# Optimization experiments

Hardware: AMD Instinct MI355X
Metric: run time of the kernel (lower is better)

The kernel has to match this reference:

```python
import jax, jax.numpy as jnp
import numpy as np

B, L, DM, E, N, R, S = 2, 1024, 512, 1024, 16, 32, 64
BN_SCALE = float(1.0 / np.sqrt(1.0 + 1e-5))  # eval-mode BatchNorm1d with default running stats


def _ssm(x, Wx, bx, Wdt, bdt, A_log, D):
    # x: [B,L,E] -> Mamba selective scan output [B,L,E]
    dbc = x @ Wx.T + bx                                   # [B,L,R+2N]
    delta = jax.nn.softplus(dbc[..., :R] @ Wdt.T + bdt)   # [B,L,E]
    Bm = dbc[..., R:R + N]                                # [B,L,N]
    Cm = dbc[..., R + N:]                                 # [B,L,N]
    A = -jnp.exp(A_log)                                   # [E,N]
    dA = jnp.exp(delta[..., None] * A)                    # [B,L,E,N]
    dBx = delta[..., None] * Bm[:, :, None, :] * x[..., None]

    def comb(c1, c2):
        a1, b1 = c1
        a2, b2 = c2
        return a1 * a2, b1 * a2 + b2

    _, h = jax.lax.associative_scan(comb, (dA, dBx), axis=1)  # [B,L,E,N]
    return jnp.einsum('blen,bln->ble', h, Cm) + D * x


def _gmask_idx(length, batch):
    ref = (length + 1) // 2
    idx = jnp.arange(length, dtype=jnp.float32)
    sigma = jnp.abs(idx - ref).mean()
    w = jnp.exp(-0.5 * (idx - ref) ** 2 / sigma ** 2)
    w = w / w.sum()
    return jnp.broadcast_to(w, (batch, length))


def _gmask_vec(seq):
    length = seq.shape[1]
    ref = seq[:, (length + 1) // 2, :]
    d = jnp.linalg.norm(seq - ref[:, None, :], axis=2)    # [B,L]
    sigma = d.mean(axis=1, keepdims=True)
    w = jnp.exp(-0.5 * (d / sigma) ** 2)
    return w / w.sum(axis=1, keepdims=True)


def _spatial_attn(x, w, b):
    # x: [B,L,C]; SpatialAttention: returns weighted map in [B,C,L] layout
    xt = jnp.swapaxes(x, 1, 2)                            # [B,C,L]
    fmap = (w[0] * xt.max(axis=1) + w[1] * xt.mean(axis=1) + b) * BN_SCALE
    wmap = jax.nn.sigmoid(jax.nn.relu(fmap))[:, None, :]  # [B,1,L]
    return xt * wmap                                      # [B,C,L]


def _forward(x, W_in_x, b_in_x, W_in_z, b_in_z, convf_w, convf_b, convb_w, convb_b,
             Wx_f, bx_f, Wdt_f, bdt_f, A_log_f, D_f,
             Wx_b, bx_b, Wdt_b, bdt_b, A_log_b, D_b,
             W_cat, b_cat, sa_w, sa_b, wA_f, wV_f,
             W_proj, b_proj, W_Bi, b_Bi, tf_w, tf_b, W_out, b_out):
    b_, l_, _ = x.shape
    xi = x @ W_in_x.T + b_in_x                            # [B,L,E]
    z = x @ W_in_z.T + b_in_z                             # [B,L,E]
    # depthwise conv1d with kernel_size=1 == per-channel affine
    x_f = jax.nn.silu(xi * convf_w + convf_b)
    x_b = jax.nn.silu(jnp.flip(xi, axis=1) * convb_w + convb_b)
    y_f = jnp.tanh(_ssm(x_f, Wx_f, bx_f, Wdt_f, bdt_f, A_log_f, D_f))
    y_b = jnp.tanh(_ssm(x_b, Wx_b, bx_b, Wdt_b, bdt_b, A_log_b, D_b))
    gi = _gmask_idx(l_, b_)
    mf = jax.nn.softmax(gi * _gmask_vec(y_f), axis=1)
    mb = jax.nn.softmax(gi * _gmask_vec(y_b), axis=1)
    y_cat = jnp.concatenate([y_f * mf[..., None],
                             y_b * jnp.flip(mb[..., None], axis=1)], axis=-1)
    y = y_cat @ W_cat.T + b_cat                           # [B,L,E]
    m = jax.nn.softmax(gi * _gmask_vec(y_cat), axis=1)
    y = y * m[..., None]
    yw = _spatial_attn(y, sa_w, sa_b)                     # [B,E,L]
    y = jnp.swapaxes(yw, 1, 2)                            # [B,L,E]
    # STL tokenizer (forward direction weights)
    Aw = jax.nn.softmax(jnp.swapaxes(y @ wA_f.T, 1, 2), axis=-1)  # [B,S,L]
    u = Aw @ (y @ wV_f)                                   # [B,S,E]
    # z branch: adaptive average pool L -> S (L % S == 0), then SiLU
    zp = jax.nn.silu(jnp.swapaxes(z, 1, 2).reshape(b_, E, S, l_ // S).mean(-1))
    zt = jnp.swapaxes(zp, 1, 2)                           # [B,S,E]
    # TokenFuser -- faithful to original's .view-based memory reinterpretation
    Y = (u.reshape(b_, E, S) @ W_proj.T + b_proj).reshape(b_, S, E)
    Bw = jax.nn.sigmoid(zt @ W_Bi.T + b_Bi)               # [B,S,S]
    BwY = Bw @ Y                                          # [B,S,E]
    xj = _spatial_attn(zt, tf_w, tf_b).reshape(b_, S, E)  # view (reshape), not transpose
    out = BwY + xj
    return jnp.tanh(out @ W_out.T + b_out)                # [B,S,DM]


def setup_inputs():
    ks = jax.random.split(jax.random.key(0), 24)
    g = lambda i, shape, s=0.02: jax.random.normal(ks[i], shape, dtype=jnp.float32) * s
    A_log = jnp.log(jnp.tile(jnp.arange(1, N + 1, dtype=jnp.float32), (E, 1)))
    return dict(
        x=jax.random.normal(ks[0], (B, L, DM), dtype=jnp.float32),
        W_in_x=g(1, (E, DM)), b_in_x=jnp.zeros((E,), jnp.float32),
        W_in_z=g(2, (E, DM)), b_in_z=jnp.zeros((E,), jnp.float32),
        convf_w=1.0 + g(3, (E,)), convf_b=jnp.zeros((E,), jnp.float32),
        convb_w=1.0 + g(4, (E,)), convb_b=jnp.zeros((E,), jnp.float32),
        Wx_f=g(5, (R + 2 * N, E)), bx_f=jnp.zeros((R + 2 * N,), jnp.float32),
        Wdt_f=g(6, (E, R)), bdt_f=jnp.full((E,), -4.0, jnp.float32),
        A_log_f=A_log, D_f=jnp.ones((E,), jnp.float32),
        Wx_b=g(7, (R + 2 * N, E)), bx_b=jnp.zeros((R + 2 * N,), jnp.float32),
        Wdt_b=g(8, (E, R)), bdt_b=jnp.full((E,), -4.0, jnp.float32),
        A_log_b=A_log, D_b=jnp.ones((E,), jnp.float32),
        W_cat=g(9, (E, 2 * E)), b_cat=jnp.zeros((E,), jnp.float32),
        sa_w=g(10, (2,), 0.5), sa_b=jnp.zeros((), jnp.float32),
        wA_f=g(11, (S, E), 0.05), wV_f=g(12, (E, E), 0.02),
        W_proj=g(13, (S, S), 0.1), b_proj=jnp.zeros((S,), jnp.float32),
        W_Bi=g(14, (S, E)), b_Bi=jnp.zeros((S,), jnp.float32),
        tf_w=g(15, (2,), 0.5), tf_b=jnp.zeros((), jnp.float32),
        W_out=g(16, (DM, E)), b_out=jnp.zeros((DM,), jnp.float32),
    )


def reference(x, W_in_x, b_in_x, W_in_z, b_in_z, convf_w, convf_b, convb_w, convb_b,
              Wx_f, bx_f, Wdt_f, bdt_f, A_log_f, D_f,
              Wx_b, bx_b, Wdt_b, bdt_b, A_log_b, D_b,
              W_cat, b_cat, sa_w, sa_b, wA_f, wV_f,
              W_proj, b_proj, W_Bi, b_Bi, tf_w, tf_b, W_out, b_out):
    return _forward(x, W_in_x, b_in_x, W_in_z, b_in_z, convf_w, convf_b, convb_w, convb_b,
                    Wx_f, bx_f, Wdt_f, bdt_f, A_log_f, D_f,
                    Wx_b, bx_b, Wdt_b, bdt_b, A_log_b, D_b,
                    W_cat, b_cat, sa_w, sa_b, wA_f, wV_f,
                    W_proj, b_proj, W_Bi, b_Bi, tf_w, tf_b, W_out, b_out)
```

## Files before the change

kernel.cpp:

```cpp
#include <hip/hip_runtime.h>
#include <math.h>

#define DEVI static __device__ __forceinline__

namespace {

constexpr float BN_SCALE_C = 0.9999950000374997f;

typedef __bf16 bf8v __attribute__((ext_vector_type(8)));
typedef float f4v __attribute__((ext_vector_type(4)));

DEVI float sigmoidf_(float x){ return 1.0f/(1.0f+expf(-x)); }
DEVI float siluf_(float x){ return x/(1.0f+expf(-x)); }
DEVI float softplusf_(float x){ return fmaxf(x,0.0f) + log1pf(expf(-fabsf(x))); }

DEVI unsigned short f2bf(float f){
  union{float f; unsigned int u;} v; v.f=f;
  unsigned int r = v.u + 0x7fffu + ((v.u>>16)&1u);
  return (unsigned short)(r>>16);
}
DEVI float bf2f(unsigned short u){
  union{unsigned int u; float f;} v; v.u = ((unsigned int)u)<<16;
  return v.f;
}

DEVI float bredw_sum(float v, float* sh){
  #pragma unroll
  for (int o=32;o;o>>=1) v += __shfl_xor(v, o);
  __syncthreads();
  if ((threadIdx.x&63)==0) sh[threadIdx.x>>6] = v;
  __syncthreads();
  return sh[0]+sh[1]+sh[2]+sh[3];
}
DEVI float bredw_max(float v, float* sh){
  #pragma unroll
  for (int o=32;o;o>>=1) v = fmaxf(v, __shfl_xor(v, o));
  __syncthreads();
  if ((threadIdx.x&63)==0) sh[threadIdx.x>>6] = v;
  __syncthreads();
  return fmaxf(fmaxf(sh[0],sh[1]), fmaxf(sh[2],sh[3]));
}

DEVI void gld_lds16(const unsigned short* g, unsigned short* l){
  __builtin_amdgcn_global_load_lds(
      (const __attribute__((address_space(1))) unsigned int*)(g),
      (__attribute__((address_space(3))) unsigned int*)(l), 16, 0, 0);
}

DEVI void stage_tile64(const unsigned short* __restrict__ Ak,
                       const unsigned short* __restrict__ Bk,
                       size_t lda, size_t ldb,
                       unsigned short* As, unsigned short* Bs,
                       int w, int lane)
{
  #pragma unroll
  for (int i=0;i<2;++i){
    int seg = (w<<1) + i;
    int row = (seg<<3) + (lane>>3);
    int c   = (lane & 7) ^ (row & 7);
    gld_lds16(Ak + (size_t)row*lda + (c<<3), As + (seg<<9));
    gld_lds16(Bk + (size_t)row*ldb + (c<<3), Bs + (seg<<9));
  }
}

DEVI void gemm_core(const unsigned short* __restrict__ Ag,
                    const unsigned short* __restrict__ Bg,
                    size_t lda, size_t ldb, int ksteps,
                    unsigned short* As, unsigned short* Bs, f4v (&acc)[2][2])
{
  const int tid = threadIdx.x;
  const int lane = tid & 63, w = tid >> 6;
  const int wr = w >> 1, wc = w & 1;
  const int l15 = lane & 15, l4 = lane >> 4;

  int cur = 0;
  stage_tile64(Ag, Bg, lda, ldb, As, Bs, w, lane);
  asm volatile("s_waitcnt vmcnt(0)" ::: "memory");
  __syncthreads();
  for (int ks = 0; ks < ksteps; ++ks){
    unsigned short* Asc = As + (cur<<12);
    unsigned short* Bsc = Bs + (cur<<12);
    if (ks+1 < ksteps)
      stage_tile64(Ag + (size_t)(ks+1)*64, Bg + (size_t)(ks+1)*64, lda, ldb,
                   As + ((cur^1)<<12), Bs + ((cur^1)<<12), w, lane);
    #pragma unroll
    for (int kk=0;kk<2;++kk){
      int cb = (kk<<2) + l4;
      bf8v af[2], bfv[2];
      #pragma unroll
      for (int mi=0;mi<2;++mi){
        int row = (wr<<5)+(mi<<4)+l15;
        af[mi] = *(const bf8v*)(Asc + (row<<6) + ((cb^(row&7))<<3));
      }
      #pragma unroll
      for (int ni=0;ni<2;++ni){
        int row = (wc<<5)+(ni<<4)+l15;
        bfv[ni] = *(const bf8v*)(Bsc + (row<<6) + ((cb^(row&7))<<3));
      }
      #pragma unroll
      for (int mi=0;mi<2;++mi)
        #pragma unroll
        for (int ni=0;ni<2;++ni)
          acc[mi][ni] = __builtin_amdgcn_mfma_f32_16x16x32_bf16(af[mi], bfv[ni], acc[mi][ni], 0,0,0);
    }
    asm volatile("s_waitcnt vmcnt(0)" ::: "memory");
    __syncthreads();
    cur ^= 1;
  }
}

__global__ __launch_bounds__(256) void gemm_bf16_k(
    const unsigned short* __restrict__ A, const unsigned short* __restrict__ Bt,
    const float* __restrict__ bias, float* __restrict__ C,
    int N, int K,
    const unsigned short* __restrict__ Bt2, const float* __restrict__ bias2, long sC)
{
  __shared__ unsigned short As[8192], Bs[8192];
  if (Bt2 && blockIdx.z){ Bt = Bt2; bias = bias2; C += sC; }
  const int m0 = blockIdx.y<<6, n0 = blockIdx.x<<6;
  f4v acc[2][2] = {};
  gemm_core(A + (size_t)m0*K, Bt + (size_t)n0*K, K, K, K>>6, As, Bs, acc);
  const int lane = threadIdx.x & 63, w = threadIdx.x >> 6;
  const int wr = w>>1, wc = w&1, l15 = lane&15, l4 = lane>>4;
  #pragma unroll
  for (int mi=0;mi<2;++mi)
    #pragma unroll
    for (int ni=0;ni<2;++ni){
      int col = n0 + (wc<<5) + (ni<<4) + l15;
      float bv = bias ? bias[col] : 0.f;
      #pragma unroll
      for (int r=0;r<4;++r){
        int rowg = m0 + (wr<<5) + (mi<<4) + (l4<<2) + r;
        C[(size_t)rowg*N + col] = acc[mi][ni][r] + bv;
      }
    }
}

__global__ __launch_bounds__(256) void gemm_bf16_splitk_k(
    const unsigned short* __restrict__ A, const unsigned short* __restrict__ Bt,
    float* __restrict__ P, int N, int K, int KC, int mshift, long sB)
{
  __shared__ unsigned short As[8192], Bs[8192];
  const int m0 = blockIdx.y<<6, n0 = blockIdx.x<<6, ch = blockIdx.z;
  const unsigned short* Bb = Bt + (size_t)(m0>>mshift)*sB;
  f4v acc[2][2] = {};
  gemm_core(A + (size_t)m0*K + (size_t)ch*KC, Bb + (size_t)n0*K + (size_t)ch*KC,
            K, K, KC>>6, As, Bs, acc);
  const size_t Mtot = (size_t)gridDim.y<<6;
  float* Pc = P + (size_t)ch*Mtot*N;
  const int lane = threadIdx.x & 63, w = threadIdx.x >> 6;
  const int wr = w>>1, wc = w&1, l15 = lane&15, l4 = lane>>4;
  #pragma unroll
  for (int mi=0;mi<2;++mi)
    #pragma unroll
    for (int ni=0;ni<2;++ni){
      int col = n0 + (wc<<5) + (ni<<4) + l15;
      #pragma unroll
      for (int r=0;r<4;++r){
        int rowg = m0 + (wr<<5) + (mi<<4) + (l4<<2) + r;
        Pc[(size_t)rowg*N + col] = acc[mi][ni][r];
      }
    }
}

template<int ACT>
__global__ __launch_bounds__(256) void sk_reduce_k(
    const float* __restrict__ P, const float* __restrict__ b0,
    int nshift, int MN, int nch, float* __restrict__ out)
{
  int i = blockIdx.x*256 + threadIdx.x;
  if (i >= MN) return;
  float s = 0.f;
  for (int c=0;c<nch;++c) s += P[(size_t)c*MN + i];
  if (b0) s += b0[i & ((1<<nshift)-1)];
  if (ACT==3) s = tanhf(s);
  out[i] = s;
}

__global__ __launch_bounds__(256) void skred_bf_k(const float* __restrict__ P,
                                                  unsigned short* __restrict__ out)
{
  int i = (blockIdx.x*256 + threadIdx.x)<<2;
  float4 s0 = *(const float4*)(P + i);
  float4 s1 = *(const float4*)(P + 131072 + i);
  float4 s2 = *(const float4*)(P + 262144 + i);
  float4 s3 = *(const float4*)(P + 393216 + i);
  union{unsigned short u[4]; uint2 p;} o;
  o.u[0] = f2bf(s0.x+s1.x+s2.x+s3.x);
  o.u[1] = f2bf(s0.y+s1.y+s2.y+s3.y);
  o.u[2] = f2bf(s0.z+s1.z+s2.z+s3.z);
  o.u[3] = f2bf(s0.w+s1.w+s2.w+s3.w);
  *(uint2*)(out + i) = o.p;
}

__global__ __launch_bounds__(256) void castall_k(
    const float* __restrict__ s0, unsigned short* __restrict__ d0, int n0,
    const float* __restrict__ s1, unsigned short* __restrict__ d1, int n1,
    const float* __restrict__ s2, unsigned short* __restrict__ d2, int n2,
    const float* __restrict__ s3, unsigned short* __restrict__ d3, int n3,
    const float* __restrict__ s4, unsigned short* __restrict__ d4, int n4,
    const float* __restrict__ s5, unsigned short* __restrict__ d5, int n5,
    const float* __restrict__ s6, unsigned short* __restrict__ d6, int n6,
    const float* __restrict__ s7, unsigned short* __restrict__ d7, int n7)
{
  int i = (blockIdx.x*256 + threadIdx.x)*4;
  const float* s; unsigned short* d;
  if (i < n0){ s = s0; d = d0; }
  else if ((i -= n0) < n1){ s = s1; d = d1; }
  else if ((i -= n1) < n2){ s = s2; d = d2; }
  else if ((i -= n2) < n3){ s = s3; d = d3; }
  else if ((i -= n3) < n4){ s = s4; d = d4; }
  else if ((i -= n4) < n5){ s = s5; d = d5; }
  else if ((i -= n5) < n6){ s = s6; d = d6; }
  else if ((i -= n6) < n7){ s = s7; d = d7; }
  else return;
  float4 v = *(const float4*)(s + i);
  union{ unsigned short u[4]; uint2 p; } o;
  o.u[0]=f2bf(v.x); o.u[1]=f2bf(v.y); o.u[2]=f2bf(v.z); o.u[3]=f2bf(v.w);
  *(uint2*)(d + i) = o.p;
}

__global__ __launch_bounds__(256) void castTw_k(const float* __restrict__ wV,
    unsigned short* __restrict__ wVT,
    const float* __restrict__ Wdt_f, const float* __restrict__ Wdt_b,
    float* __restrict__ WdtT)
{
  __shared__ float t[32][33];
  int by = blockIdx.y, bx = blockIdx.x;
  int tx = threadIdx.x & 31, ty = threadIdx.x >> 5;
  if (by < 32){
    #pragma unroll
    for (int r=0;r<4;++r){
      int row = by*32 + ty + r*8;
      t[ty + r*8][tx] = wV[(long)row*1024 + bx*32 + tx];
    }
    __syncthreads();
    #pragma unroll
    for (int r=0;r<4;++r){
      int row = bx*32 + ty + r*8;
      wVT[(long)row*1024 + by*32 + tx] = f2bf(t[tx][ty + r*8]);
    }
  } else {
    int dir = by - 32;
    const float* src = dir ? Wdt_b : Wdt_f;
    float* dst = WdtT + (dir<<15);
    #pragma unroll
    for (int r=0;r<4;++r){
      int row = bx*32 + ty + r*8;
      t[ty + r*8][tx] = src[(long)row*32 + tx];
    }
    __syncthreads();
    #pragma unroll
    for (int r=0;r<4;++r){
      int c = ty + r*8;
      dst[(long)c*1024 + bx*32 + tx] = t[tx][c];
    }
  }
}

__global__ __launch_bounds__(256) void castTbf_k(const unsigned short* __restrict__ src,
                                                 unsigned short* __restrict__ dst)
{
  __shared__ unsigned short t[32][33];
  size_t bo = (size_t)blockIdx.z << 20;
  int bx = blockIdx.x, by = blockIdx.y;
  int tx = threadIdx.x & 31, ty = threadIdx.x >> 5;
  #pragma unroll
  for (int r=0;r<4;++r){
    int row = by*32 + ty + r*8;
    t[ty + r*8][tx] = src[bo + (long)row*1024 + bx*32 + tx];
  }
  __syncthreads();
  #pragma unroll
  for (int r=0;r<4;++r){
    int row = bx*32 + ty + r*8;
    dst[bo + (long)row*1024 + by*32 + tx] = t[tx][ty + r*8];
  }
}

__global__ __launch_bounds__(256) void convzt_k(const float* __restrict__ xi, const float* __restrict__ z,
    const float* __restrict__ cfw, const float* __restrict__ cfb,
    const float* __restrict__ cbw, const float* __restrict__ cbb,
    float* __restrict__ xf, float* __restrict__ xb, unsigned short* __restrict__ xfb_bf,
    float* __restrict__ ztb)
{
  int bx = blockIdx.x, t = threadIdx.x;
  if (bx < 2048){
    int base = (bx*256 + t) << 2;
    int e = base & 1023;
    int bl = base >> 10; int l = bl & 1023, b = bl >> 10;
    float4 cw = *(const float4*)(cfw + e);
    float4 cb = *(const float4*)(cfb + e);
    float4 xv = *(const float4*)(xi + base);
    float4 vf;
    vf.x = siluf_(fmaf(xv.x, cw.x, cb.x));
    vf.y = siluf_(fmaf(xv.y, cw.y, cb.y));
    vf.z = siluf_(fmaf(xv.z, cw.z, cb.z));
    vf.w = siluf_(fmaf(xv.w, cw.w, cb.w));
    *(float4*)(xf + base) = vf;
    union{unsigned short u[4]; uint2 p;} o;
    o.u[0]=f2bf(vf.x); o.u[1]=f2bf(vf.y); o.u[2]=f2bf(vf.z); o.u[3]=f2bf(vf.w);
    *(uint2*)(xfb_bf + base) = o.p;
    int jb = (((b<<10) + (1023-l))<<10) + e;
    float4 cw2 = *(const float4*)(cbw + e);
    float4 cb2 = *(const float4*)(cbb + e);
    float4 xw = *(const float4*)(xi + jb);
    float4 vb;
    vb.x = siluf_(fmaf(xw.x, cw2.x, cb2.x));
    vb.y = siluf_(fmaf(xw.y, cw2.y, cb2.y));
    vb.z = siluf_(fmaf(xw.z, cw2.z, cb2.z));
    vb.w = siluf_(fmaf(xw.w, cw2.w, cb2.w));
    *(float4*)(xb + base) = vb;
    union{unsigned short u[4]; uint2 p;} o2;
    o2.u[0]=f2bf(vb.x); o2.u[1]=f2bf(vb.y); o2.u[2]=f2bf(vb.z); o2.u[3]=f2bf(vb.w);
    *(uint2*)(xfb_bf + 2097152 + base) = o2.p;
  } else {
    int base = ((bx-2048)*256 + t) << 2;
    int e = base & 1023; int bs = base >> 10; int s = bs & 63; int b = bs >> 6;
    const float* zp = z + (((long)((b<<10)+(s<<4)))<<10) + e;
    float4 sm = {0.f,0.f,0.f,0.f};
    #pragma unroll
    for (int j=0;j<16;++j){
      float4 v = *(const float4*)(zp + ((long)j<<10));
      sm.x += v.x; sm.y += v.y; sm.z += v.z; sm.w += v.w;
    }
    float4 o;
    o.x = siluf_(sm.x*(1.f/16.f)); o.y = siluf_(sm.y*(1.f/16.f));
    o.z = siluf_(sm.z*(1.f/16.f)); o.w = siluf_(sm.w*(1.f/16.f));
    *(float4*)(ztb + base) = o;
  }
}

__global__ __launch_bounds__(256) void dbcdelta_k(
    const float* __restrict__ Pd,
    const float* __restrict__ bx_f, const float* __restrict__ bx_b,
    const float* __restrict__ WdtT,
    const float* __restrict__ bdt_f, const float* __restrict__ bdt_b,
    float* __restrict__ dbcF, float* __restrict__ delta)
{
  __shared__ float sdbc[8][64];
  const int t = threadIdx.x;
  const int r0 = blockIdx.x * 8;
  const int dir = r0 >> 11;
  const float* bx  = dir ? bx_b  : bx_f;
  const float* bdt = dir ? bdt_b : bdt_f;
  const float* WT  = WdtT + (dir<<15);
  for (int idx=t; idx<512; idx+=256){
    int r = idx>>6, c = idx&63;
    long a = (long)(r0+r)*64 + c;
    float s = Pd[a] + Pd[262144+a] + Pd[524288+a] + Pd[786432+a] + bx[c];
    sdbc[r][c] = s;
    dbcF[a] = s;
  }
  __syncthreads();
  const int c0 = t << 2;
  float4 bv = *(const float4*)(bdt + c0);
  float4 acc[8];
  #pragma unroll
  for (int r=0;r<8;++r) acc[r] = bv;
  #pragma unroll
  for (int k=0;k<32;++k){
    float4 w = *(const float4*)(WT + (k<<10) + c0);
    #pragma unroll
    for (int r=0;r<8;++r){
      float a = sdbc[r][k];
      acc[r].x = fmaf(a, w.x, acc[r].x);
      acc[r].y = fmaf(a, w.y, acc[r].y);
      acc[r].z = fmaf(a, w.z, acc[r].z);
      acc[r].w = fmaf(a, w.w, acc[r].w);
    }
  }
  #pragma unroll
  for (int r=0;r<8;++r){
    float4 o;
    o.x = softplusf_(acc[r].x); o.y = softplusf_(acc[r].y);
    o.z = softplusf_(acc[r].z); o.w = softplusf_(acc[r].w);
    *(float4*)(delta + (long)(r0+r)*1024 + c0) = o;
  }
}

__global__ __launch_bounds__(256) void ssm_chunk_k(
    const float* __restrict__ xs0, const float* __restrict__ dl0,
    const float* __restrict__ dbc0, const float* __restrict__ A_log_f,
    const float* __restrict__ A_log_b,
    float* __restrict__ pA0, float* __restrict__ hend0)
{
  const int dir = blockIdx.y;
  const float* xs   = xs0  + (size_t)dir*2097152;
  const float* delta= dl0  + (size_t)dir*2097152;
  const float* dbc  = dbc0 + (size_t)dir*131072;
  const float* A_log= dir ? A_log_b : A_log_f;
  float* pA   = pA0   + (size_t)dir*1048576;
  float* hend = hend0 + (size_t)dir*1048576;

  __shared__ float sB[32][16];
  int g = blockIdx.x*256 + threadIdx.x;
  int e = g & 1023;
  int bc = g >> 10;
  int c = bc & 31, b = bc >> 5;
  for (int i=threadIdx.x; i<512; i+=256){
    int l=i>>4, n=i&15;
    sB[l][n] = dbc[(((b<<10) + (c<<5) + l)<<6) + 32 + n];
  }
  __syncthreads();
  float An[16];
  #pragma unroll
  for (int n=0;n<16;++n) An[n] = -__expf(A_log[(e<<4)+n]);
  float h[16], p[16];
  #pragma unroll
  for (int n=0;n<16;++n){ h[n]=0.0f; p[n]=1.0f; }
  long base = ((long)((b<<10) + (c<<5)))*1024 + e;
  for (int l=0;l<32;++l){
    float dl = delta[base + ((long)l<<10)];
    float xv = xs[base + ((long)l<<10)];
    float dx = dl*xv;
    #pragma unroll
    for (int n=0;n<16;++n){
      float a = __expf(dl*An[n]);
      h[n] = fmaf(a, h[n], dx*sB[l][n]);
      p[n] *= a;
    }
  }
  long ob = ((long)((b<<5)+c)<<4)*1024 + e;
  #pragma unroll
  for (int n=0;n<16;++n){ pA[ob + ((long)n<<10)] = p[n]; hend[ob + ((long)n<<10)] = h[n]; }
}

__global__ __launch_bounds__(256) void ssm_carry_k(
    const float* __restrict__ pA, const float* __restrict__ hend, float* __restrict__ Hc)
{
  int i = blockIdx.x*256 + threadIdx.x;
  int e = i & 1023, n = (i>>10)&15, b = (i>>14)&1, dir = (i>>15)&1;
  const float* pAd = pA   + (size_t)dir*1048576;
  const float* hd  = hend + (size_t)dir*1048576;
  float* Hd        = Hc   + (size_t)dir*1048576;
// ... 100 lines not shown
    float* __restrict__ mfG, float* __restrict__ mbG, float* __restrict__ mvG)
{
  __shared__ float mfs[1024], mbs[1024], sh[4];
  const int b = blockIdx.x, t = threadIdx.x;
  const float nf512 = nrm[(b<<10)+512];
  const float nb512 = nrm[2048+(b<<10)+512];
  float gi[4], nf[4], pf[4], nb[4], pb[4];
  float gs = 0.f;
  #pragma unroll
  for (int i=0;i<4;++i){
    int l = t + (i<<8);
    float q = (float)(l-512) * (1.0f/256.0f);
    gi[i] = __expf(-0.5f*q*q); gs += gi[i];
    nf[i] = nrm[(b<<10)+l];      pf[i] = dotv[(b<<10)+l];
    nb[i] = nrm[2048+(b<<10)+l]; pb[i] = dotv[2048+(b<<10)+l];
  }
  float gsum = bredw_sum(gs, sh);
  float mf[4], mb[4], d[4];
  #pragma unroll
  for (int i=0;i<4;++i) d[i] = sqrtf(fmaxf(nf[i] - 2.f*pf[i] + nf512, 0.f));
  softmask(d, gi, gsum, sh, mf);
  #pragma unroll
  for (int i=0;i<4;++i) d[i] = sqrtf(fmaxf(nb[i] - 2.f*pb[i] + nb512, 0.f));
  softmask(d, gi, gsum, sh, mb);
  #pragma unroll
  for (int i=0;i<4;++i){
    int l = t + (i<<8);
    mfs[l] = mf[i]; mbs[l] = mb[i];
    mfG[(b<<10)+l] = mf[i]; mbG[(b<<10)+l] = mb[i];
  }
  __syncthreads();
  const float mf512 = mfs[512], mb511 = mbs[511];
  #pragma unroll
  for (int i=0;i<4;++i){
    int l = t + (i<<8);
    float mbf = mbs[1023-l];
    float dc2 = mf[i]*mf[i]*nf[i] - 2.f*mf[i]*mf512*pf[i] + mf512*mf512*nf512
              + mbf*mbf*nb[i]     - 2.f*mbf*mb511*pb[i]   + mb511*mb511*nb512;
    d[i] = sqrtf(fmaxf(dc2, 0.f));
  }
  float mv[4];
  softmask(d, gi, gsum, sh, mv);
  #pragma unroll
  for (int i=0;i<4;++i) mvG[(b<<10)+t+(i<<8)] = mv[i];
}

__global__ __launch_bounds__(256) void ycat_k(const float* __restrict__ yf, const float* __restrict__ yb,
    const float* __restrict__ mf, const float* __restrict__ mb, unsigned short* __restrict__ yc)
{
  int base = (blockIdx.x*256 + threadIdx.x) << 2;
  int e = base & 1023; int bl = base >> 10; int l = bl & 1023, b = bl >> 10;
  float mfv = mf[bl];
  float mbv = mb[(b<<10) + (1023-l)];
  float4 vf = *(const float4*)(yf + base);
  float4 vb = *(const float4*)(yb + base);
  long r = (long)bl*2048;
  union{unsigned short u[4]; uint2 p;} o;
  o.u[0]=f2bf(vf.x*mfv); o.u[1]=f2bf(vf.y*mfv); o.u[2]=f2bf(vf.z*mfv); o.u[3]=f2bf(vf.w*mfv);
  *(uint2*)(yc + r + e) = o.p;
  union{unsigned short u[4]; uint2 p;} o2;
  o2.u[0]=f2bf(vb.x*mbv); o2.u[1]=f2bf(vb.y*mbv); o2.u[2]=f2bf(vb.z*mbv); o2.u[3]=f2bf(vb.w*mbv);
  *(uint2*)(yc + r + 1024 + e) = o2.p;
}

__global__ __launch_bounds__(256) void rowscale_k(const float* __restrict__ y, const float* __restrict__ m,
    const float* __restrict__ sw, const float* __restrict__ sb, unsigned short* __restrict__ yo)
{
  __shared__ float sh[4];
  int row = blockIdx.x;
  float mv = m[row];
  float4 v = ((const float4*)(y + (long)row*1024))[threadIdx.x];
  v.x *= mv; v.y *= mv; v.z *= mv; v.w *= mv;
  float mx = fmaxf(fmaxf(v.x,v.y), fmaxf(v.z,v.w));
  float sm = v.x+v.y+v.z+v.w;
  float rmax = bredw_max(mx, sh);
  float rsum = bredw_sum(sm, sh);
  float fmap = (sw[0]*rmax + sw[1]*(rsum*(1.0f/1024.0f)) + sb[0])*BN_SCALE_C;
  float sc = sigmoidf_(fmaxf(fmap, 0.0f));
  union{unsigned short u[4]; uint2 p;} o;
  o.u[0]=f2bf(v.x*sc); o.u[1]=f2bf(v.y*sc); o.u[2]=f2bf(v.z*sc); o.u[3]=f2bf(v.w*sc);
  *(uint2*)(yo + (long)row*1024 + (threadIdx.x<<2)) = o.p;
}

__global__ __launch_bounds__(256) void awsm_part_k(const float* __restrict__ P2,
                                                   unsigned short* __restrict__ Aw)
{
  __shared__ float sh[4];
  int bs = blockIdx.x; int b = bs >> 6, s = bs & 63;
  float v[4]; float mx=-1e30f;
  #pragma unroll
  for(int i=0;i<4;++i){
    int l = threadIdx.x+(i<<8);
    long a = (long)((b<<10)+l)*64 + s;
    float sv = 0.f;
    #pragma unroll
    for (int ch=0; ch<8; ++ch) sv += P2[(long)ch*131072 + a];
    v[i] = sv; mx = fmaxf(mx, sv);
  }
  mx = bredw_max(mx, sh);
  float sm=0.0f;
  #pragma unroll
  for(int i=0;i<4;++i){ v[i]=__expf(v[i]-mx); sm+=v[i]; }
  sm = bredw_sum(sm, sh);
  float inv = 1.0f/sm;
  #pragma unroll
  for(int i=0;i<4;++i){ int l=threadIdx.x+(i<<8); Aw[(((b<<6)+s)<<10)+l] = f2bf(v[i]*inv); }
}

__global__ __launch_bounds__(256) void upbw_k(const float* __restrict__ P2u,
    const float* __restrict__ W_proj, const float* __restrict__ b_proj,
    const float* __restrict__ zt, const float* __restrict__ W_Bi,
    const float* __restrict__ b_Bi, const float* __restrict__ tw,
    const float* __restrict__ tb,
    float* __restrict__ Yp, float* __restrict__ Bw, float* __restrict__ gz)
{
  __shared__ float a[1024];
  __shared__ float sh[4];
  const int t = threadIdx.x;
  if (blockIdx.x < 256){
    const int r0 = blockIdx.x*8;
    for (int idx=t; idx<512; idx+=256){
      int r = idx>>6, sp = idx&63;
      long ad = (long)(r0+r)*64 + sp;
      float s = P2u[ad] + P2u[131072+ad] + P2u[262144+ad] + P2u[393216+ad];
      a[idx] = s;
    }
    __syncthreads();
    int r = t >> 5, c = t & 31;
    const float* ar = a + (r<<6);
    float acc1 = b_proj[c], acc2 = b_proj[c+32];
    for (int sp=0; sp<64; ++sp){
      float av = ar[sp];
      acc1 = fmaf(av, W_proj[c*64+sp], acc1);
      acc2 = fmaf(av, W_proj[(c+32)*64+sp], acc2);
    }
    long row = r0 + r;
    Yp[row*64 + c] = acc1;
    Yp[row*64 + c + 32] = acc2;
  } else {
    const int row = blockIdx.x - 256;
    float4 zv = ((const float4*)(zt + (long)row*1024))[t];
    *(float4*)(a + (t<<2)) = zv;
    float mx = fmaxf(fmaxf(zv.x,zv.y), fmaxf(zv.z,zv.w));
    float sm = zv.x+zv.y+zv.z+zv.w;
    mx = bredw_max(mx, sh);
    sm = bredw_sum(sm, sh);
    if (t==0){
      float f = (tw[0]*mx + tw[1]*(sm*(1.0f/1024.0f)) + tb[0])*BN_SCALE_C;
      gz[row] = sigmoidf_(fmaxf(f,0.0f));
    }
    __syncthreads();
    int col = t >> 2, q = t & 3;
    const float4* wp = (const float4*)(W_Bi + (long)col*1024 + q*256);
    const float4* zp = (const float4*)(a + q*256);
    float acc = 0.f;
    for (int i=0;i<64;++i){
      float4 w = wp[i], zc = zp[i];
      acc += w.x*zc.x + w.y*zc.y + w.z*zc.z + w.w*zc.w;
    }
    acc += __shfl_xor(acc, 1);
    acc += __shfl_xor(acc, 2);
    if (q==0) Bw[(long)row*64 + col] = sigmoidf_(acc + b_Bi[col]);
  }
}

__global__ __launch_bounds__(256) void o_k(const float* __restrict__ Bw,
    const float* __restrict__ Yp, const float* __restrict__ zt,
    const float* __restrict__ gz, unsigned short* __restrict__ O_bf)
{
  __shared__ float bwrow[64];
  const int t = threadIdx.x;
  const int bs = blockIdx.x; const int b = bs >> 6, s = bs & 63;
  if (t < 64) bwrow[t] = Bw[(long)bs*64 + t];
  __syncthreads();
  const int e0 = t << 2;
  const float* yb = Yp + (long)b*65536 + e0;
  float4 acc = {0.f,0.f,0.f,0.f};
  for (int s2=0; s2<64; ++s2){
    float f = bwrow[s2];
    float4 y = *(const float4*)(yb + ((long)s2<<10));
    acc.x = fmaf(f,y.x,acc.x); acc.y = fmaf(f,y.y,acc.y);
    acc.z = fmaf(f,y.z,acc.z); acc.w = fmaf(f,y.w,acc.w);
  }
  int ez = (s<<4) + (e0>>6);
  float o4[4] = {acc.x, acc.y, acc.z, acc.w};
  union{unsigned short u[4]; uint2 p;} o;
  #pragma unroll
  for (int k=0;k<4;++k){
    int sz = (e0&63) + k;
    float xj = zt[(((long)((b<<6)+sz))<<10) + ez] * gz[(b<<6)+sz];
    o.u[k] = f2bf(o4[k] + xj);
  }
  *(uint2*)(O_bf + (long)bs*1024 + e0) = o.p;
}

}

extern "C" void kernel_launch(void* const* d_in, const int* in_sizes, int n_in,
                              void* d_out, int out_size, void* d_ws, size_t ws_size,
                              hipStream_t stream)
{
  (void)in_sizes; (void)n_in; (void)out_size; (void)ws_size;
  const float* x      = (const float*)d_in[0];
  const float* W_in_x = (const float*)d_in[1];
  const float* b_in_x = (const float*)d_in[2];
  const float* W_in_z = (const float*)d_in[3];
  const float* b_in_z = (const float*)d_in[4];
  const float* cfw    = (const float*)d_in[5];
  const float* cfb    = (const float*)d_in[6];
  const float* cbw    = (const float*)d_in[7];
  const float* cbb    = (const float*)d_in[8];
  const float* Wx_f   = (const float*)d_in[9];
  const float* bx_f   = (const float*)d_in[10];
  const float* Wdt_f  = (const float*)d_in[11];
  const float* bdt_f  = (const float*)d_in[12];
  const float* A_log_f= (const float*)d_in[13];
  const float* D_f    = (const float*)d_in[14];
  const float* Wx_b   = (const float*)d_in[15];
  const float* bx_b   = (const float*)d_in[16];
  const float* Wdt_b  = (const float*)d_in[17];
  const float* bdt_b  = (const float*)d_in[18];
  const float* A_log_b= (const float*)d_in[19];
  const float* D_b    = (const float*)d_in[20];
  const float* W_cat  = (const float*)d_in[21];
  const float* b_cat  = (const float*)d_in[22];
  const float* sa_w   = (const float*)d_in[23];
  const float* sa_b   = (const float*)d_in[24];
  const float* wA_f   = (const float*)d_in[25];
  const float* wV_f   = (const float*)d_in[26];
  const float* W_proj = (const float*)d_in[27];
  const float* b_proj = (const float*)d_in[28];
  const float* W_Bi   = (const float*)d_in[29];
  const float* b_Bi   = (const float*)d_in[30];
  const float* tf_w   = (const float*)d_in[31];
  const float* tf_b   = (const float*)d_in[32];
  const float* W_out  = (const float*)d_in[33];
  const float* b_out  = (const float*)d_in[34];
  float* out = (float*)d_out;
  float* ws  = (float*)d_ws;

  const size_t M1 = 1u<<20;
  float* xi = ws;
  float* pA = ws;
  unsigned short* ycat_bf = (unsigned short*)ws;
  float* z = ws + 2*M1;
  float* hend = ws + 2*M1;
  float* ybufF = ws + 2*M1;
  float* xf = ws + 4*M1;
  unsigned short* ybuf_bf = (unsigned short*)(ws + 4*M1);
  float* xb = ws + 6*M1;
  unsigned short* ybufT_bf = (unsigned short*)(ws + 6*M1);
  float* yf = ws + 8*M1;
  float* yb = ws + 10*M1;
  float* P2 = ws + 10*M1;
  float* P2b = P2 + 524288;
  unsigned short* xfxb_bf = (unsigned short*)(ws + 12*M1);
  float* deltaF = ws + 12*M1;
  float* Pd = ws + 16*M1;
  unsigned short* x_bf = (unsigned short*)(ws + 17*M1);
  float* Hc = ws + 16*M1;
  float* dbcF = ws + 18*M1;
  size_t woff = 18*M1 + 262144;
  unsigned short* Winx_bf = (unsigned short*)(ws + woff); woff += 262144;
  unsigned short* Winz_bf = (unsigned short*)(ws + woff); woff += 262144;
  unsigned short* Wcat_bf = (unsigned short*)(ws + woff); woff += M1;
  unsigned short* wVT_bf  = (unsigned short*)(ws + woff); woff += 524288;
  unsigned short* wA_bf   = (unsigned short*)(ws + woff); woff += 32768;
  unsigned short* Wx_bf   = (unsigned short*)(ws + woff); woff += 65536;
  unsigned short* Wout_bf = (unsigned short*)(ws + woff); woff += 262144;
  float* WdtT = ws + woff; woff += 65536;
  float* ztb  = ws + woff; woff += 131072;
  float* nrm  = ws + woff; woff += 4096;
  float* dotv = ws + woff; woff += 4096;
  float* mfG  = ws + woff; woff += 2048;
  float* mbG  = ws + woff; woff += 2048;
  float* mvG  = ws + woff; woff += 2048;
  float* gz   = ws + woff; woff += 256;
  unsigned short* Aw_bf = (unsigned short*)(ws + woff); woff += 65536;
  unsigned short* uR_bf = (unsigned short*)(ws + woff); woff += 65536;
  float* Yp   = ws + woff; woff += 131072;
  float* Bw   = ws + woff; woff += 8192;
  unsigned short* O_bf = (unsigned short*)(ws + woff); woff += 65536;

  dim3 blk(256);

  castall_k<<<4800,blk,0,stream>>>(x, x_bf, 1048576,
                                   W_in_x, Winx_bf, 524288,
                                   W_in_z, Winz_bf, 524288,
                                   W_cat, Wcat_bf, 2097152,
                                   wA_f, wA_bf, 65536,
                                   Wx_f, Wx_bf, 65536,
                                   Wx_b, Wx_bf + 65536, 65536,
                                   W_out, Wout_bf, 524288);
  castTw_k<<<dim3(32,34),blk,0,stream>>>(wV_f, wVT_bf, Wdt_f, Wdt_b, WdtT);

  gemm_bf16_k<<<dim3(16,32,2),blk,0,stream>>>(x_bf, Winx_bf, b_in_x, xi, 1024, 512,
                                              Winz_bf, b_in_z, (long)(2*M1));
  convzt_k<<<2176,blk,0,stream>>>(xi, z, cfw,cfb,cbw,cbb, xf, xb, xfxb_bf, ztb);

  gemm_bf16_splitk_k<<<dim3(1,64,4),blk,0,stream>>>(xfxb_bf, Wx_bf, Pd, 64, 1024, 256, 11, 65536);
  dbcdelta_k<<<512,blk,0,stream>>>(Pd, bx_f, bx_b, WdtT, bdt_f, bdt_b, dbcF, deltaF);

  ssm_chunk_k<<<dim3(256,2),blk,0,stream>>>(xf, deltaF, dbcF, A_log_f, A_log_b, pA, hend);
  ssm_carry_k<<<256,blk,0,stream>>>(pA, hend, Hc);
  ssm_out_k<<<dim3(256,2),blk,0,stream>>>(xf, deltaF, dbcF, A_log_f, A_log_b, Hc, D_f, D_b, yf);

  stats_k<<<4096,blk,0,stream>>>(yf, nrm, dotv);
  mask2_k<<<2,blk,0,stream>>>(nrm, dotv, mfG, mbG, mvG);
  ycat_k<<<2048,blk,0,stream>>>(yf, yb, mfG, mbG, ycat_bf);

  gemm_bf16_k<<<dim3(16,32,1),blk,0,stream>>>(ycat_bf, Wcat_bf, b_cat, ybufF, 1024, 2048,
                                              nullptr, nullptr, 0);
  rowscale_k<<<2048,blk,0,stream>>>(ybufF, mvG, sa_w, sa_b, ybuf_bf);

  gemm_bf16_splitk_k<<<dim3(1,32,8),blk,0,stream>>>(ybuf_bf, wA_bf, P2, 64, 1024, 128, 31, 0);
  awsm_part_k<<<128,blk,0,stream>>>(P2, Aw_bf);
  castTbf_k<<<dim3(32,32,2),blk,0,stream>>>(ybuf_bf, ybufT_bf);
  gemm_bf16_splitk_k<<<dim3(16,2,4),blk,0,stream>>>(Aw_bf, ybufT_bf, P2, 1024, 1024, 256, 6, 1048576);
  skred_bf_k<<<128,blk,0,stream>>>(P2, uR_bf);
  gemm_bf16_splitk_k<<<dim3(16,2,4),blk,0,stream>>>(uR_bf, wVT_bf, P2b, 1024, 1024, 256, 31, 0);

  upbw_k<<<384,blk,0,stream>>>(P2b, W_proj, b_proj, ztb, W_Bi, b_Bi, tf_w, tf_b, Yp, Bw, gz);
  o_k<<<128,blk,0,stream>>>(Bw, Yp, ztb, gz, O_bf);

  gemm_bf16_splitk_k<<<dim3(8,2,8),blk,0,stream>>>(O_bf, Wout_bf, P2, 512, 1024, 128, 31, 0);
  sk_reduce_k<3><<<256,blk,0,stream>>>(P2, b_out, 9, 65536, 8, out);
}
```

Before: 216.3 us.

## Replace split-K GEMMs with full-K GEMMs using fused epilogues and merge transpose kernels

Removes the split-K partial-sum buffers and their reduce kernels. Each GEMM now computes the full K in one launch and applies bias, bf16 conversion or tanh in its epilogue. The weight transposes are folded into the cast kernel and the ybuf transpose into the softmax kernel, reducing the number of kernel launches and intermediate memory traffic. The trade-off is much smaller grids for several GEMMs, which lowers parallelism on a wide GPU.

```diff
diff --git a/kernel.cpp b/kernel.cpp
--- a/kernel.cpp
+++ b/kernel.cpp
@@ -18,10 +18,6 @@
   union{float f; unsigned int u;} v; v.f=f;
   unsigned int r = v.u + 0x7fffu + ((v.u>>16)&1u);
   return (unsigned short)(r>>16);
-}
-DEVI float bf2f(unsigned short u){
-  union{unsigned int u; float f;} v; v.u = ((unsigned int)u)<<16;
-  return v.f;
 }
 
 DEVI float bredw_sum(float v, float* sh){
@@ -109,17 +105,21 @@
   }
 }
 
+template<int EPI>
 __global__ __launch_bounds__(256) void gemm_bf16_k(
     const unsigned short* __restrict__ A, const unsigned short* __restrict__ Bt,
-    const float* __restrict__ bias, float* __restrict__ C,
+    const float* __restrict__ bias, void* __restrict__ Cout,
     int N, int K,
-    const unsigned short* __restrict__ Bt2, const float* __restrict__ bias2, long sC)
+    const unsigned short* __restrict__ Bt2, const float* __restrict__ bias2, long sC,
+    int mshift, long sB)
 {
   __shared__ unsigned short As[8192], Bs[8192];
-  if (Bt2 && blockIdx.z){ Bt = Bt2; bias = bias2; C += sC; }
+  float* Cf = (float*)Cout;
+  if (Bt2 && blockIdx.z){ Bt = Bt2; bias = bias2; Cf += sC; }
   const int m0 = blockIdx.y<<6, n0 = blockIdx.x<<6;
+  const unsigned short* Bb = Bt + (size_t)(m0>>mshift)*sB;
   f4v acc[2][2] = {};
-  gemm_core(A + (size_t)m0*K, Bt + (size_t)n0*K, K, K, K>>6, As, Bs, acc);
+  gemm_core(A + (size_t)m0*K, Bb + (size_t)n0*K, K, K, K>>6, As, Bs, acc);
   const int lane = threadIdx.x & 63, w = threadIdx.x >> 6;
   const int wr = w>>1, wc = w&1, l15 = lane&15, l4 = lane>>4;
   #pragma unroll
@@ -127,70 +127,46 @@
     #pragma unroll
     for (int ni=0;ni<2;++ni){
       int col = n0 + (wc<<5) + (ni<<4) + l15;
-      float bv = bias ? bias[col] : 0.f;
+      float bv = (EPI!=1 && bias) ? bias[col] : 0.f;
       #pragma unroll
       for (int r=0;r<4;++r){
         int rowg = m0 + (wr<<5) + (mi<<4) + (l4<<2) + r;
-        C[(size_t)rowg*N + col] = acc[mi][ni][r] + bv;
+        float v = acc[mi][ni][r] + bv;
+        if (EPI==1){
+          ((unsigned short*)Cout)[(size_t)rowg*N + col] = f2bf(v);
+        } else {
+          if (EPI==2) v = tanhf(v);
+          Cf[(size_t)rowg*N + col] = v;
+        }
       }
     }
 }
 
-__global__ __launch_bounds__(256) void gemm_bf16_splitk_k(
-    const unsigned short* __restrict__ A, const unsigned short* __restrict__ Bt,
-    float* __restrict__ P, int N, int K, int KC, int mshift, long sB)
+__global__ __launch_bounds__(256) void gemm_dbc_k(
+    const unsigned short* __restrict__ A, const unsigned short* __restrict__ Wx_bf,
+    const float* __restrict__ bx_f, const float* __restrict__ bx_b,
+    float* __restrict__ dbcF)
 {
   __shared__ unsigned short As[8192], Bs[8192];
-  const int m0 = blockIdx.y<<6, n0 = blockIdx.x<<6, ch = blockIdx.z;
-  const unsigned short* Bb = Bt + (size_t)(m0>>mshift)*sB;
+  const int m0 = blockIdx.y<<6;
+  const int dir = m0 >> 11;
   f4v acc[2][2] = {};
-  gemm_core(A + (size_t)m0*K + (size_t)ch*KC, Bb + (size_t)n0*K + (size_t)ch*KC,
-            K, K, KC>>6, As, Bs, acc);
-  const size_t Mtot = (size_t)gridDim.y<<6;
-  float* Pc = P + (size_t)ch*Mtot*N;
+  gemm_core(A + (size_t)m0*1024, Wx_bf + (size_t)dir*65536, 1024, 1024, 16, As, Bs, acc);
+  const float* bx = dir ? bx_b : bx_f;
   const int lane = threadIdx.x & 63, w = threadIdx.x >> 6;
   const int wr = w>>1, wc = w&1, l15 = lane&15, l4 = lane>>4;
   #pragma unroll
   for (int mi=0;mi<2;++mi)
     #pragma unroll
     for (int ni=0;ni<2;++ni){
-      int col = n0 + (wc<<5) + (ni<<4) + l15;
+      int col = (wc<<5) + (ni<<4) + l15;
+      float bv = bx[col];
       #pragma unroll
       for (int r=0;r<4;++r){
         int rowg = m0 + (wr<<5) + (mi<<4) + (l4<<2) + r;
-        Pc[(size_t)rowg*N + col] = acc[mi][ni][r];
+        dbcF[(size_t)rowg*64 + col] = acc[mi][ni][r] + bv;
       }
     }
-}
-
-template<int ACT>
-__global__ __launch_bounds__(256) void sk_reduce_k(
-    const float* __restrict__ P, const float* __restrict__ b0,
-    int nshift, int MN, int nch, float* __restrict__ out)
-{
-  int i = blockIdx.x*256 + threadIdx.x;
-  if (i >= MN) return;
-  float s = 0.f;
-  for (int c=0;c<nch;++c) s += P[(size_t)c*MN + i];
-  if (b0) s += b0[i & ((1<<nshift)-1)];
-  if (ACT==3) s = tanhf(s);
-  out[i] = s;
-}
-
-__global__ __launch_bounds__(256) void skred_bf_k(const float* __restrict__ P,
-                                                  unsigned short* __restrict__ out)
-{
-  int i = (blockIdx.x*256 + threadIdx.x)<<2;
-  float4 s0 = *(const float4*)(P + i);
-  float4 s1 = *(const float4*)(P + 131072 + i);
-  float4 s2 = *(const float4*)(P + 262144 + i);
-  float4 s3 = *(const float4*)(P + 393216 + i);
-  union{unsigned short u[4]; uint2 p;} o;
-  o.u[0] = f2bf(s0.x+s1.x+s2.x+s3.x);
-  o.u[1] = f2bf(s0.y+s1.y+s2.y+s3.y);
-  o.u[2] = f2bf(s0.z+s1.z+s2.z+s3.z);
-  o.u[3] = f2bf(s0.w+s1.w+s2.w+s3.w);
-  *(uint2*)(out + i) = o.p;
 }
 
 __global__ __launch_bounds__(256) void castall_k(
@@ -201,8 +177,47 @@
     const float* __restrict__ s4, unsigned short* __restrict__ d4, int n4,
     const float* __restrict__ s5, unsigned short* __restrict__ d5, int n5,
     const float* __restrict__ s6, unsigned short* __restrict__ d6, int n6,
-    const float* __restrict__ s7, unsigned short* __restrict__ d7, int n7)
-{
+    const float* __restrict__ s7, unsigned short* __restrict__ d7, int n7,
+    const float* __restrict__ wV, unsigned short* __restrict__ wVT,
+    const float* __restrict__ Wdt_f, const float* __restrict__ Wdt_b,
+    float* __restrict__ WdtT)
+{
+  __shared__ float tsh[32][33];
+  if (blockIdx.x >= 4800){
+    int tb = blockIdx.x - 4800;
+    int tx = threadIdx.x & 31, ty = threadIdx.x >> 5;
+    if (tb < 1024){
+      int by = tb >> 5, bx = tb & 31;
+      #pragma unroll
+      for (int r=0;r<4;++r){
+        int row = by*32 + ty + r*8;
+        tsh[ty + r*8][tx] = wV[(long)row*1024 + bx*32 + tx];
+      }
+      __syncthreads();
+      #pragma unroll
+      for (int r=0;r<4;++r){
+        int row = bx*32 + ty + r*8;
+        wVT[(long)row*1024 + by*32 + tx] = f2bf(tsh[tx][ty + r*8]);
+      }
+    } else {
+      int q = tb - 1024;
+      int dir = q >> 5, bi = q & 31;
+      const float* src = dir ? Wdt_b : Wdt_f;
+      float* dst = WdtT + (dir<<15);
+      #pragma unroll
+      for (int r=0;r<4;++r){
+        int row = bi*32 + ty + r*8;
+        tsh[ty + r*8][tx] = src[(long)row*32 + tx];
+      }
+      __syncthreads();
+      #pragma unroll
+      for (int r=0;r<4;++r){
+        int c = ty + r*8;
+        dst[(long)c*1024 + bi*32 + tx] = tsh[tx][c];
+      }
+    }
+    return;
+  }
   int i = (blockIdx.x*256 + threadIdx.x)*4;
   const float* s; unsigned short* d;
   if (i < n0){ s = s0; d = d0; }
@@ -218,64 +233,6 @@
   union{ unsigned short u[4]; uint2 p; } o;
   o.u[0]=f2bf(v.x); o.u[1]=f2bf(v.y); o.u[2]=f2bf(v.z); o.u[3]=f2bf(v.w);
   *(uint2*)(d + i) = o.p;
-}
-
-__global__ __launch_bounds__(256) void castTw_k(const float* __restrict__ wV,
-    unsigned short* __restrict__ wVT,
-    const float* __restrict__ Wdt_f, const float* __restrict__ Wdt_b,
-    float* __restrict__ WdtT)
-{
-  __shared__ float t[32][33];
-  int by = blockIdx.y, bx = blockIdx.x;
-  int tx = threadIdx.x & 31, ty = threadIdx.x >> 5;
-  if (by < 32){
-    #pragma unroll
-    for (int r=0;r<4;++r){
-      int row = by*32 + ty + r*8;
-      t[ty + r*8][tx] = wV[(long)row*1024 + bx*32 + tx];
-    }
-    __syncthreads();
-    #pragma unroll
-    for (int r=0;r<4;++r){
-      int row = bx*32 + ty + r*8;
-      wVT[(long)row*1024 + by*32 + tx] = f2bf(t[tx][ty + r*8]);
-    }
-  } else {
-    int dir = by - 32;
-    const float* src = dir ? Wdt_b : Wdt_f;
-    float* dst = WdtT + (dir<<15);
-    #pragma unroll
-    for (int r=0;r<4;++r){
-      int row = bx*32 + ty + r*8;
-      t[ty + r*8][tx] = src[(long)row*32 + tx];
-    }
-    __syncthreads();
-    #pragma unroll
-    for (int r=0;r<4;++r){
-      int c = ty + r*8;
-      dst[(long)c*1024 + bx*32 + tx] = t[tx][c];
-    }
-  }
-}
-
-__global__ __launch_bounds__(256) void castTbf_k(const unsigned short* __restrict__ src,
-                                                 unsigned short* __restrict__ dst)
-{
-  __shared__ unsigned short t[32][33];
-  size_t bo = (size_t)blockIdx.z << 20;
-  int bx = blockIdx.x, by = blockIdx.y;
-  int tx = threadIdx.x & 31, ty = threadIdx.x >> 5;
-  #pragma unroll
-  for (int r=0;r<4;++r){
-    int row = by*32 + ty + r*8;
-    t[ty + r*8][tx] = src[bo + (long)row*1024 + bx*32 + tx];
-  }
-  __syncthreads();
-  #pragma unroll
-  for (int r=0;r<4;++r){
-    int row = bx*32 + ty + r*8;
-    dst[bo + (long)row*1024 + by*32 + tx] = t[tx][ty + r*8];
-  }
 }
 
 __global__ __launch_bounds__(256) void convzt_k(const float* __restrict__ xi, const float* __restrict__ z,
@@ -332,25 +289,19 @@
 }
 
 __global__ __launch_bounds__(256) void dbcdelta_k(
-    const float* __restrict__ Pd,
-    const float* __restrict__ bx_f, const float* __restrict__ bx_b,
-    const float* __restrict__ WdtT,
+    const float* __restrict__ dbcF, const float* __restrict__ WdtT,
     const float* __restrict__ bdt_f, const float* __restrict__ bdt_b,
-    float* __restrict__ dbcF, float* __restrict__ delta)
+    float* __restrict__ delta)
 {
   __shared__ float sdbc[8][64];
   const int t = threadIdx.x;
   const int r0 = blockIdx.x * 8;
   const int dir = r0 >> 11;
-  const float* bx  = dir ? bx_b  : bx_f;
   const float* bdt = dir ? bdt_b : bdt_f;
   const float* WT  = WdtT + (dir<<15);
   for (int idx=t; idx<512; idx+=256){
     int r = idx>>6, c = idx&63;
-    long a = (long)(r0+r)*64 + c;
-    float s = Pd[a] + Pd[262144+a] + Pd[524288+a] + Pd[786432+a] + bx[c];
-    sdbc[r][c] = s;
-    dbcF[a] = s;
+    sdbc[r][c] = dbcF[(long)(r0+r)*64 + c];
   }
   __syncthreads();
   const int c0 = t << 2;
@@ -617,32 +568,50 @@
   *(uint2*)(yo + (long)row*1024 + (threadIdx.x<<2)) = o.p;
 }
 
-__global__ __launch_bounds__(256) void awsm_part_k(const float* __restrict__ P2,
-                                                   unsigned short* __restrict__ Aw)
+__global__ __launch_bounds__(256) void awsmT_k(const float* __restrict__ yA,
+    unsigned short* __restrict__ Aw,
+    const unsigned short* __restrict__ src, unsigned short* __restrict__ dst)
 {
   __shared__ float sh[4];
-  int bs = blockIdx.x; int b = bs >> 6, s = bs & 63;
-  float v[4]; float mx=-1e30f;
-  #pragma unroll
-  for(int i=0;i<4;++i){
-    int l = threadIdx.x+(i<<8);
-    long a = (long)((b<<10)+l)*64 + s;
-    float sv = 0.f;
-    #pragma unroll
-    for (int ch=0; ch<8; ++ch) sv += P2[(long)ch*131072 + a];
-    v[i] = sv; mx = fmaxf(mx, sv);
-  }
-  mx = bredw_max(mx, sh);
-  float sm=0.0f;
-  #pragma unroll
-  for(int i=0;i<4;++i){ v[i]=__expf(v[i]-mx); sm+=v[i]; }
-  sm = bredw_sum(sm, sh);
-  float inv = 1.0f/sm;
-  #pragma unroll
-  for(int i=0;i<4;++i){ int l=threadIdx.x+(i<<8); Aw[(((b<<6)+s)<<10)+l] = f2bf(v[i]*inv); }
-}
-
-__global__ __launch_bounds__(256) void upbw_k(const float* __restrict__ P2u,
+  __shared__ unsigned short tsh[32][33];
+  if (blockIdx.x < 128){
+    int bs = blockIdx.x; int b = bs >> 6, s = bs & 63;
+    float v[4]; float mx=-1e30f;
+    #pragma unroll
+    for(int i=0;i<4;++i){
+      int l = threadIdx.x+(i<<8);
+      v[i] = yA[(long)((b<<10)+l)*64 + s];
+      mx = fmaxf(mx, v[i]);
+    }
+    mx = bredw_max(mx, sh);
+    float sm=0.0f;
+    #pragma unroll
+    for(int i=0;i<4;++i){ v[i]=__expf(v[i]-mx); sm+=v[i]; }
+    sm = bredw_sum(sm, sh);
+    float inv = 1.0f/sm;
+    #pragma unroll
+    for(int i=0;i<4;++i){ int l=threadIdx.x+(i<<8); Aw[(((b<<6)+s)<<10)+l] = f2bf(v[i]*inv); }
+  } else {
+    int tb = blockIdx.x - 128;
+    size_t bo = (size_t)(tb>>10) << 20;
+    int rem = tb & 1023;
+    int by = rem >> 5, bx = rem & 31;
+    int tx = threadIdx.x & 31, ty = threadIdx.x >> 5;
+    #pragma unroll
+    for (int r=0;r<4;++r){
+      int row = by*32 + ty + r*8;
+      tsh[ty + r*8][tx] = src[bo + (long)row*1024 + bx*32 + tx];
+    }
+    __syncthreads();
+    #pragma unroll
+    for (int r=0;r<4;++r){
+      int row = bx*32 + ty + r*8;
+      dst[bo + (long)row*1024 + by*32 + tx] = tsh[tx][ty + r*8];
+    }
+  }
+}
+
+__global__ __launch_bounds__(256) void upbw_k(const float* __restrict__ u2f,
     const float* __restrict__ W_proj, const float* __restrict__ b_proj,
     const float* __restrict__ zt, const float* __restrict__ W_Bi,
     const float* __restrict__ b_Bi, const float* __restrict__ tw,
@@ -656,9 +625,7 @@
     const int r0 = blockIdx.x*8;
     for (int idx=t; idx<512; idx+=256){
       int r = idx>>6, sp = idx&63;
-      long ad = (long)(r0+r)*64 + sp;
-      float s = P2u[ad] + P2u[131072+ad] + P2u[262144+ad] + P2u[393216+ad];
-      a[idx] = s;
+      a[idx] = u2f[(long)(r0+r)*64 + sp];
     }
     __syncthreads();
     int r = t >> 5, c = t & 31;
@@ -787,11 +754,9 @@
   unsigned short* ybufT_bf = (unsigned short*)(ws + 6*M1);
   float* yf = ws + 8*M1;
   float* yb = ws + 10*M1;
-  float* P2 = ws + 10*M1;
-  float* P2b = P2 + 524288;
+  float* u2f = ws + 10*M1;
   unsigned short* xfxb_bf = (unsigned short*)(ws + 12*M1);
   float* deltaF = ws + 12*M1;
-  float* Pd = ws + 16*M1;
   unsigned short* x_bf = (unsigned short*)(ws + 17*M1);
   float* Hc = ws + 16*M1;
   float* dbcF = ws + 18*M1;
@@ -811,6 +776,7 @@
   float* mbG  = ws + woff; woff += 2048;
   float* mvG  = ws + woff; woff += 2048;
   float* gz   = ws + woff; woff += 256;
+  float* yA   = ws + woff; woff += 131072;
   unsigned short* Aw_bf = (unsigned short*)(ws + woff); woff += 65536;
   unsigned short* uR_bf = (unsigned short*)(ws + woff); woff += 65536;
   float* Yp   = ws + woff; woff += 131072;
@@ -819,22 +785,22 @@
 
   dim3 blk(256);
 
-  castall_k<<<4800,blk,0,stream>>>(x, x_bf, 1048576,
+  castall_k<<<5888,blk,0,stream>>>(x, x_bf, 1048576,
                                    W_in_x, Winx_bf, 524288,
                                    W_in_z, Winz_bf, 524288,
                                    W_cat, Wcat_bf, 2097152,
                                    wA_f, wA_bf, 65536,
                                    Wx_f, Wx_bf, 65536,
                                    Wx_b, Wx_bf + 65536, 65536,
-                                   W_out, Wout_bf, 524288);
-  castTw_k<<<dim3(32,34),blk,0,stream>>>(wV_f, wVT_bf, Wdt_f, Wdt_b, WdtT);
-
-  gemm_bf16_k<<<dim3(16,32,2),blk,0,stream>>>(x_bf, Winx_bf, b_in_x, xi, 1024, 512,
-                                              Winz_bf, b_in_z, (long)(2*M1));
+                                   W_out, Wout_bf, 524288,
+                                   wV_f, wVT_bf, Wdt_f, Wdt_b, WdtT);
+
+  gemm_bf16_k<0><<<dim3(16,32,2),blk,0,stream>>>(x_bf, Winx_bf, b_in_x, xi, 1024, 512,
+                                                 Winz_bf, b_in_z, (long)(2*M1), 31, 0);
   convzt_k<<<2176,blk,0,stream>>>(xi, z, cfw,cfb,cbw,cbb, xf, xb, xfxb_bf, ztb);
 
-  gemm_bf16_splitk_k<<<dim3(1,64,4),blk,0,stream>>>(xfxb_bf, Wx_bf, Pd, 64, 1024, 256, 11, 65536);
-  dbcdelta_k<<<512,blk,0,stream>>>(Pd, bx_f, bx_b, WdtT, bdt_f, bdt_b, dbcF, deltaF);
+  gemm_dbc_k<<<dim3(1,64),blk,0,stream>>>(xfxb_bf, Wx_bf, bx_f, bx_b, dbcF);
+  dbcdelta_k<<<512,blk,0,stream>>>(dbcF, WdtT, bdt_f, bdt_b, deltaF);
 
   ssm_chunk_k<<<dim3(256,2),blk,0,stream>>>(xf, deltaF, dbcF, A_log_f, A_log_b, pA, hend);
   ssm_carry_k<<<256,blk,0,stream>>>(pA, hend, Hc);
@@ -844,20 +810,21 @@
   mask2_k<<<2,blk,0,stream>>>(nrm, dotv, mfG, mbG, mvG);
   ycat_k<<<2048,blk,0,stream>>>(yf, yb, mfG, mbG, ycat_bf);
 
-  gemm_bf16_k<<<dim3(16,32,1),blk,0,stream>>>(ycat_bf, Wcat_bf, b_cat, ybufF, 1024, 2048,
-                                              nullptr, nullptr, 0);
+  gemm_bf16_k<0><<<dim3(16,32,1),blk,0,stream>>>(ycat_bf, Wcat_bf, b_cat, ybufF, 1024, 2048,
+                                                 nullptr, nullptr, 0, 31, 0);
   rowscale_k<<<2048,blk,0,stream>>>(ybufF, mvG, sa_w, sa_b, ybuf_bf);
 
-  gemm_bf16_splitk_k<<<dim3(1,32,8),blk,0,stream>>>(ybuf_bf, wA_bf, P2, 64, 1024, 128, 31, 0);
-  awsm_part_k<<<128,blk,0,stream>>>(P2, Aw_bf);
-  castTbf_k<<<dim3(32,32,2),blk,0,stream>>>(ybuf_bf, ybufT_bf);
-  gemm_bf16_splitk_k<<<dim3(16,2,4),blk,0,stream>>>(Aw_bf, ybufT_bf, P2, 1024, 1024, 256, 6, 1048576);
-  skred_bf_k<<<128,blk,0,stream>>>(P2, uR_bf);
-  gemm_bf16_splitk_k<<<dim3(16,2,4),blk,0,stream>>>(uR_bf, wVT_bf, P2b, 1024, 1024, 256, 31, 0);
-
-  upbw_k<<<384,blk,0,stream>>>(P2b, W_proj, b_proj, ztb, W_Bi, b_Bi, tf_w, tf_b, Yp, Bw, gz);
+  gemm_bf16_k<0><<<dim3(1,32,1),blk,0,stream>>>(ybuf_bf, wA_bf, nullptr, yA, 64, 1024,
+                                                nullptr, nullptr, 0, 31, 0);
+  awsmT_k<<<2176,blk,0,stream>>>(yA, Aw_bf, ybuf_bf, ybufT_bf);
+  gemm_bf16_k<1><<<dim3(16,2,1),blk,0,stream>>>(Aw_bf, ybufT_bf, nullptr, uR_bf, 1024, 1024,
+                                                nullptr, nullptr, 0, 6, (long)M1);
+  gemm_bf16_k<0><<<dim3(16,2,1),blk,0,stream>>>(uR_bf, wVT_bf, nullptr, u2f, 1024, 1024,
+                                                nullptr, nullptr, 0, 31, 0);
+
+  upbw_k<<<384,blk,0,stream>>>(u2f, W_proj, b_proj, ztb, W_Bi, b_Bi, tf_w, tf_b, Yp, Bw, gz);
   o_k<<<128,blk,0,stream>>>(Bw, Yp, ztb, gz, O_bf);
 
-  gemm_bf16_splitk_k<<<dim3(8,2,8),blk,0,stream>>>(O_bf, Wout_bf, P2, 512, 1024, 128, 31, 0);
-  sk_reduce_k<3><<<256,blk,0,stream>>>(P2, b_out, 9, 65536, 8, out);
-}
+  gemm_bf16_k<2><<<dim3(8,2,1),blk,0,stream>>>(O_bf, Wout_bf, b_out, out, 512, 1024,
+                                               nullptr, nullptr, 0, 31, 0);
+}
```

Result: slower. 229.4 us (+6.1%).
